# Kernel optimization log

Hardware: AMD Instinct MI355X
Metric: run time of the kernel (lower is better)

The kernel has to match this reference:

```python
import jax, jax.numpy as jnp
import numpy as np

GROUPS = 32
EPS = 1e-5


def _group_norm(x, w, b):
    B, C, H, W = x.shape
    xr = x.reshape(B, GROUPS, C // GROUPS, H, W)
    mean = xr.mean(axis=(2, 3, 4), keepdims=True)
    var = xr.var(axis=(2, 3, 4), keepdims=True)
    xn = ((xr - mean) * jax.lax.rsqrt(var + EPS)).reshape(B, C, H, W)
    return xn * w[None, :, None, None] + b[None, :, None, None]


def _conv1x1(w, b, x):
    # 1x1 conv == per-pixel channel matmul
    return jnp.einsum('oc,bchw->bohw', w, x) + b[None, :, None, None]


def setup_inputs() -> dict:
    key = jax.random.key(0)
    ks = jax.random.split(key, 6)
    C = 512
    s = 1.0 / np.sqrt(C)  # kaiming-uniform-ish scale for 1x1 convs
    return {
        'x': jax.random.normal(ks[0], (4, C, 64, 64), jnp.float32),
        'gn_w': jnp.ones((C,), jnp.float32),
        'gn_b': jnp.zeros((C,), jnp.float32),
        'qw': jax.random.normal(ks[1], (C, C), jnp.float32) * s,
        'qb': jnp.zeros((C,), jnp.float32),
        'kw': jax.random.normal(ks[2], (C, C), jnp.float32) * s,
        'kb': jnp.zeros((C,), jnp.float32),
        'vw': jax.random.normal(ks[3], (C, C), jnp.float32) * s,
        'vb': jnp.zeros((C,), jnp.float32),
        'pw': jax.random.normal(ks[4], (C, C), jnp.float32) * s,
        'pb': jnp.zeros((C,), jnp.float32),
    }


def reference(x, gn_w, gn_b, qw, qb, kw, kb, vw, vb, pw, pb):
    B, C, H, W = x.shape
    h_ = _group_norm(x, gn_w, gn_b)
    q = _conv1x1(qw, qb, h_).reshape(B, C, H * W)
    k = _conv1x1(kw, kb, h_).reshape(B, C, H * W)
    v = _conv1x1(vw, vb, h_).reshape(B, C, H * W)
    # scores [B, HW(query), HW(key)]
    scores = jnp.einsum('bcq,bck->bqk', q, k) * (C ** -0.5)
    attn = jax.nn.softmax(scores, axis=-1)
    out = jnp.einsum('bqk,bdk->bdq', attn, v).reshape(B, C, H, W)
    return x + _conv1x1(pw, pb, out)
```

## Files before the change

kernel.cpp:

```cpp
#include <hip/hip_runtime.h>

#define DEV __device__ __forceinline__

typedef __attribute__((ext_vector_type(8))) short short8;
typedef __attribute__((ext_vector_type(4))) float floatx4;
typedef __attribute__((ext_vector_type(4))) int i32x4;
typedef __attribute__((ext_vector_type(2))) long longx2;

DEV unsigned short f2bs(float x) {
    unsigned u = __float_as_uint(x);
    unsigned r = (u + 0x7fffu + ((u >> 16) & 1u)) >> 16;
    return (unsigned short)r;
}

DEV unsigned char f2fp8(float x) {
#if __has_builtin(__builtin_amdgcn_cvt_pk_fp8_f32)
    int pk = __builtin_amdgcn_cvt_pk_fp8_f32(x, 0.f, 0, false);
    return (unsigned char)(pk & 0xff);
#else
    unsigned u = __float_as_uint(x);
    unsigned s = (u >> 24) & 0x80;
    unsigned a = u & 0x7fffffff;
    unsigned um = a + 0x7ffffu + ((a >> 20) & 1u);
    unsigned r = (a >= 0x3c800000u) ? ((um >> 20) - 0x3C0u) : 0u;
    return (unsigned char)(r | s);
#endif
}

DEV unsigned pack_fp8x4(float v0, float v1, float v2, float v3) {
#if __has_builtin(__builtin_amdgcn_cvt_pk_fp8_f32)
    unsigned pk = (unsigned)__builtin_amdgcn_cvt_pk_fp8_f32(v0, v1, 0, false);
    pk = (unsigned)__builtin_amdgcn_cvt_pk_fp8_f32(v2, v3, (int)pk, true);
    return pk;
#else
    return (unsigned)f2fp8(v0) | ((unsigned)f2fp8(v1) << 8) |
           ((unsigned)f2fp8(v2) << 16) | ((unsigned)f2fp8(v3) << 24);
#endif
}

DEV unsigned pack_i8x4(float v0, float v1, float v2, float v3) {
    unsigned b0 = (unsigned)((int)rintf(v0)) & 255u;
    unsigned b1 = (unsigned)((int)rintf(v1)) & 255u;
    unsigned b2 = (unsigned)((int)rintf(v2)) & 255u;
    unsigned b3 = (unsigned)((int)rintf(v3)) & 255u;
    return b0 | (b1 << 8) | (b2 << 16) | (b3 << 24);
}

__global__ void pre_kernel(const float* __restrict__ x,
                           const float* __restrict__ qw, const float* __restrict__ kw,
                           const float* __restrict__ vw, const float* __restrict__ pw,
                           const float* __restrict__ qb, const float* __restrict__ kb,
                           unsigned short* __restrict__ wqkb, unsigned short* __restrict__ wvb,
                           unsigned short* __restrict__ wpb,
                           float* __restrict__ biasqk, float* __restrict__ rowsum,
                           float* __restrict__ stats) {
    int b = blockIdx.x, tid = threadIdx.x;
    if (b < 768) {
        const float* src = (b < 256) ? qw : (b < 512) ? kw : vw;
        unsigned short* dst = (b < 256) ? wqkb : (b < 512) ? (wqkb + 262144) : wvb;
        int off = (b & 255) * 256 + tid;
        float4 v = ((const float4*)src)[off];
        ushort4 o;
        o.x = f2bs(v.x); o.y = f2bs(v.y); o.z = f2bs(v.z); o.w = f2bs(v.w);
        ((ushort4*)dst)[off] = o;
    } else if (b < 1024) {
        int off = (b - 768) * 256 + tid;
        int row = off >> 7, c4 = (off & 127) * 4;
        float4 v = ((const float4*)pw)[off];
        float vv[4] = {v.x, v.y, v.z, v.w};
#pragma unroll
        for (int e = 0; e < 4; ++e) {
            int c = c4 + e;
            int j = (c >> 4) & 3, lc = c & 15;
            int cp = (c & ~63) | (lc * 4 + j);
            wpb[row * 512 + cp] = f2bs(vv[e]);
        }
    } else if (b == 1024) {
        biasqk[tid]       = qb[tid];
        biasqk[256 + tid] = qb[256 + tid];
        biasqk[512 + tid] = kb[tid];
        biasqk[768 + tid] = kb[256 + tid];
        float4 z = {0.f, 0.f, 0.f, 0.f};
#pragma unroll
        for (int k = 0; k < 16; ++k) ((float4*)rowsum)[k * 256 + tid] = z;
    } else {
        int bg = b - 1025;
        const float4* p = (const float4*)(x + (size_t)bg * 65536);
        float s = 0.f, ss = 0.f;
        for (int i = tid; i < 16384; i += 256) {
            float4 v = p[i];
            s += v.x + v.y + v.z + v.w;
            ss += v.x * v.x + v.y * v.y + v.z * v.z + v.w * v.w;
        }
        for (int off = 32; off; off >>= 1) { s += __shfl_down(s, off); ss += __shfl_down(ss, off); }
        __shared__ float rs[4], rss[4];
        int wave = tid >> 6, lane = tid & 63;
        if (lane == 0) { rs[wave] = s; rss[wave] = ss; }
        __syncthreads();
        if (tid == 0) {
            float S = rs[0] + rs[1] + rs[2] + rs[3];
            float SS = rss[0] + rss[1] + rss[2] + rss[3];
            float mean = S * (1.f / 65536.f);
            float var = SS * (1.f / 65536.f) - mean * mean;
            stats[bg * 2] = mean;
            stats[bg * 2 + 1] = rsqrtf(var + 1e-5f);
        }
    }
}

__global__ void gn_apply_kernel(const float* __restrict__ x, const float* __restrict__ stats,
                                const float* __restrict__ gw, const float* __restrict__ gb,
                                unsigned short* __restrict__ ht) {
    __shared__ __align__(16) unsigned short t[64][72];
    int b = blockIdx.z, c0 = blockIdx.y * 64, p0 = blockIdx.x * 64;
    int tid = threadIdx.x;
    const float* xb = x + ((size_t)b * 512 + c0) * 4096 + p0;
#pragma unroll
    for (int pass = 0; pass < 4; ++pass) {
        int cl = pass * 16 + (tid >> 4);
        int pq = (tid & 15) * 4;
        float4 v = *(const float4*)(xb + (size_t)cl * 4096 + pq);
        int c = c0 + cl, g = c >> 4;
        float mean = stats[(b * 32 + g) * 2], rstd = stats[(b * 32 + g) * 2 + 1];
        float sw = gw[c] * rstd;
        float sb = gb[c] - mean * sw;
        t[pq + 0][cl] = f2bs(v.x * sw + sb);
        t[pq + 1][cl] = f2bs(v.y * sw + sb);
        t[pq + 2][cl] = f2bs(v.z * sw + sb);
        t[pq + 3][cl] = f2bs(v.w * sw + sb);
    }
    __syncthreads();
    unsigned short* hb = ht + ((size_t)b * 4096 + p0) * 512 + c0;
#pragma unroll
    for (int pass = 0; pass < 2; ++pass) {
        int pl = pass * 32 + (tid >> 3);
        int c8 = (tid & 7) * 8;
        *(uint4*)(hb + (size_t)pl * 512 + c8) = *(const uint4*)&t[pl][c8];
    }
}

__global__ void gemm_qkv(const unsigned short* __restrict__ h_t, long long sP,
                         const unsigned short* __restrict__ wqkb,
                         const unsigned short* __restrict__ wvb,
                         char* __restrict__ q_i8, char* __restrict__ k_i8,
                         char* __restrict__ v_f8,
                         const float* __restrict__ biasqk, const float* __restrict__ vb,
                         float qs) {
    __shared__ __align__(16) unsigned short lA[128 * 64];
    __shared__ __align__(16) unsigned short lB[128 * 64];
    const int tid = threadIdx.x;
    const int wave = tid >> 6, lane = tid & 63;
    const int flat = blockIdx.x;
    const bool isqk = flat < 1024;
    int m0, n0, bz;
    const unsigned short *Ab, *Bb;
    if (isqk) {
        m0 = ((flat >> 3) & 31) * 128;
        n0 = (flat & 7) * 128;
        bz = flat >> 8;
        Ab = h_t + (size_t)bz * sP;
        Bb = wqkb;
    } else {
        const int g = flat - 1024;
        m0 = ((g >> 5) & 3) * 128;
        n0 = (g & 31) * 128;
        bz = g >> 7;
        Ab = wvb;
        Bb = h_t + (size_t)bz * sP;
    }

    floatx4 acc[4][4];
#pragma unroll
    for (int i = 0; i < 4; i++)
#pragma unroll
        for (int j = 0; j < 4; j++) acc[i][j] = (floatx4){0.f, 0.f, 0.f, 0.f};

    const int wm = (wave >> 1) * 64, wn = (wave & 1) * 64;
    const int quad = lane >> 4;
    const int lc = lane & 15;
    const int lc7 = lc & 7;

    for (int kt = 0; kt < 8; ++kt) {
        const int kbase = kt * 64;
#pragma unroll
        for (int c = 0; c < 4; ++c) {
            int d = c * 256 + tid;
            int r = d >> 3;
            int kc = (d & 7) ^ (r & 7);
            const unsigned short* ga = Ab + (size_t)(m0 + r) * 512 + kbase + kc * 8;
            const unsigned short* gb = Bb + (size_t)(n0 + r) * 512 + kbase + kc * 8;
            __builtin_amdgcn_global_load_lds(
                (const __attribute__((address_space(1))) void*)ga,
                (__attribute__((address_space(3))) void*)&lA[(size_t)(c * 256 + wave * 64) * 8], 16, 0, 0);
            __builtin_amdgcn_global_load_lds(
                (const __attribute__((address_space(1))) void*)gb,
                (__attribute__((address_space(3))) void*)&lB[(size_t)(c * 256 + wave * 64) * 8], 16, 0, 0);
        }
        __syncthreads();
#pragma unroll
        for (int kk = 0; kk < 2; ++kk) {
            const int swz = ((kk * 4 + quad) ^ lc7) * 8;
            short8 af[4], bf[4];
#pragma unroll
            for (int i = 0; i < 4; i++)
                af[i] = *(const short8*)&lA[(size_t)(wm + i * 16 + lc) * 64 + swz];
#pragma unroll
            for (int j = 0; j < 4; j++)
                bf[j] = *(const short8*)&lB[(size_t)(wn + j * 16 + lc) * 64 + swz];
#pragma unroll
            for (int i = 0; i < 4; i++)
#pragma unroll
                for (int j = 0; j < 4; j++)
                    acc[i][j] = __builtin_amdgcn_mfma_f32_16x16x32_bf16(af[i], bf[j], acc[i][j], 0, 0, 0);
        }
        __syncthreads();
    }

    const int rowb = quad * 4;
    if (isqk) {
#pragma unroll
        for (int i = 0; i < 4; i++) {
#pragma unroll
            for (int r = 0; r < 4; r++) {
                const int m = m0 + wm + i * 16 + rowb + r;
                float q[4];
#pragma unroll
                for (int j = 0; j < 4; j++) {
                    const int n = n0 + wn + j * 16 + lc;
                    q[j] = fminf(fmaxf((acc[i][j][r] + biasqk[n]) * qs, -127.f), 127.f);
                }
                const int col64 = n0 + wn;
                char* outp = (col64 < 512) ? q_i8 : k_i8;
                size_t idx = (size_t)bz * sP + (size_t)m * 512 +
                             (col64 - ((col64 < 512) ? 0 : 512)) + lc * 4;
                *(unsigned*)(outp + idx) = pack_i8x4(q[0], q[1], q[2], q[3]);
            }
        }
    } else {
#pragma unroll
        for (int i = 0; i < 4; i++) {
#pragma unroll
            for (int r = 0; r < 4; r++) {
                const int m = m0 + wm + i * 16 + rowb + r;
                const float bm = vb[m];
                float q[4];
#pragma unroll
                for (int j = 0; j < 4; j++)
                    q[j] = fminf(fmaxf(acc[i][j][r] + bm, -448.f), 448.f);
                size_t idx = (size_t)bz * sP + (size_t)m * 4096 + n0 + wn + lc * 4;
                *(unsigned*)(v_f8 + idx) = pack_fp8x4(q[0], q[1], q[2], q[3]);
            }
        }
    }
}

__global__ void gemm_proj(const unsigned short* __restrict__ A,
                          const unsigned short* __restrict__ B, long long sBb,
                          float* __restrict__ Cv, long long sCb,
                          const float* __restrict__ bias,
                          const float* __restrict__ resid, long long sRb,
                          int M, int N, int K) {
    __shared__ __align__(16) unsigned short lA[128 * 64];
    __shared__ __align__(16) unsigned short lB[128 * 64];
    const int tid = threadIdx.x;
    const int wave = tid >> 6, lane = tid & 63;
    const int m0 = blockIdx.y * 128, n0 = blockIdx.x * 128, bz = blockIdx.z;
    const unsigned short* Ab = A;
    const unsigned short* Bb = B + (size_t)bz * sBb;

    floatx4 acc[4][4];
#pragma unroll
    for (int i = 0; i < 4; i++)
#pragma unroll
        for (int j = 0; j < 4; j++) acc[i][j] = (floatx4){0.f, 0.f, 0.f, 0.f};

    const int wm = (wave >> 1) * 64, wn = (wave & 1) * 64;
    const int quad = lane >> 4;
    const int lc = lane & 15;
    const int lc7 = lc & 7;

    const int nk = K >> 6;
    for (int kt = 0; kt < nk; ++kt) {
        const int kbase = kt * 64;
#pragma unroll
        for (int c = 0; c < 4; ++c) {
            int d = c * 256 + tid;
            int r = d >> 3;
            int kc = (d & 7) ^ (r & 7);
            const unsigned short* ga = Ab + (size_t)(m0 + r) * K + kbase + kc * 8;
            const unsigned short* gb = Bb + (size_t)(n0 + r) * K + kbase + kc * 8;
            __builtin_amdgcn_global_load_lds(
                (const __attribute__((address_space(1))) void*)ga,
                (__attribute__((address_space(3))) void*)&lA[(size_t)(c * 256 + wave * 64) * 8], 16, 0, 0);
            __builtin_amdgcn_global_load_lds(
                (const __attribute__((address_space(1))) void*)gb,
                (__attribute__((address_space(3))) void*)&lB[(size_t)(c * 256 + wave * 64) * 8], 16, 0, 0);
        }
        __syncthreads();
#pragma unroll
        for (int kk = 0; kk < 2; ++kk) {
            const int swz = ((kk * 4 + quad) ^ lc7) * 8;
            short8 af[4], bf[4];
#pragma unroll
            for (int i = 0; i < 4; i++)
                af[i] = *(const short8*)&lA[(size_t)(wm + i * 16 + lc) * 64 + swz];
#pragma unroll
            for (int j = 0; j < 4; j++)
                bf[j] = *(const short8*)&lB[(size_t)(wn + j * 16 + lc) * 64 + swz];
#pragma unroll
            for (int i = 0; i < 4; i++)
#pragma unroll
                for (int j = 0; j < 4; j++)
                    acc[i][j] = __builtin_amdgcn_mfma_f32_16x16x32_bf16(af[i], bf[j], acc[i][j], 0, 0, 0);
        }
        __syncthreads();
    }

    const int rowb = quad * 4;
#pragma unroll
    for (int i = 0; i < 4; i++) {
#pragma unroll
        for (int r = 0; r < 4; r++) {
            const int m = m0 + wm + i * 16 + rowb + r;
            const float bm = bias[m];
#pragma unroll
            for (int j = 0; j < 4; j++) {
                const int n = n0 + wn + j * 16 + lc;
                size_t idx = (size_t)bz * sCb + (size_t)m * N + n;
                Cv[idx] = acc[i][j][r] + bm + resid[(size_t)bz * sRb + (size_t)m * N + n];
            }
        }
    }
}

__global__ void gemm_i8_exp(const char* __restrict__ A, long long sAb,
                            const char* __restrict__ B, long long sBb,
                            char* __restrict__ Cv, long long sCb,
                            float* __restrict__ rowsum,
                            int M, int N, int K, float scale2) {
    __shared__ __align__(16) char lA[128 * 128];
    __shared__ __align__(16) char lB[128 * 128];
    const int tid = threadIdx.x;
    const int wave = tid >> 6, lane = tid & 63;
    const int m0 = blockIdx.y * 128, n0 = blockIdx.x * 128, bz = blockIdx.z;
    const char* Ab = A + (size_t)bz * sAb;
    const char* Bb = B + (size_t)bz * sBb;

    i32x4 acc[4][4];
#pragma unroll
    for (int i = 0; i < 4; i++)
#pragma unroll
        for (int j = 0; j < 4; j++) acc[i][j] = (i32x4){0, 0, 0, 0};

    const int wm = (wave >> 1) * 64, wn = (wave & 1) * 64;
    const int quad = lane >> 4;
    const int lc = lane & 15;
    const int lc7 = lc & 7;

    const int nk = K >> 7;
    for (int kt = 0; kt < nk; ++kt) {
        const int kbase = kt * 128;
#pragma unroll
        for (int c = 0; c < 4; ++c) {
            int d = c * 256 + tid;
            int r = d >> 3;
            int kc = (d & 7) ^ (r & 7);
            const char* ga = Ab + (size_t)(m0 + r) * K + kbase + kc * 16;
            const char* gb = Bb + (size_t)(n0 + r) * K + kbase + kc * 16;
            __builtin_amdgcn_global_load_lds(
                (const __attribute__((address_space(1))) void*)ga,
                (__attribute__((address_space(3))) void*)&lA[(size_t)(c * 256 + wave * 64) * 16], 16, 0, 0);
            __builtin_amdgcn_global_load_lds(
                (const __attribute__((address_space(1))) void*)gb,
                (__attribute__((address_space(3))) void*)&lB[(size_t)(c * 256 + wave * 64) * 16], 16, 0, 0);
        }
        __syncthreads();
#pragma unroll
        for (int kk = 0; kk < 2; ++kk) {
            const int swz = ((kk * 4 + quad) ^ lc7) * 16;
            i32x4 af[4], bf[4];
#pragma unroll
            for (int i = 0; i < 4; i++)
                af[i] = *(const i32x4*)&lA[(size_t)(wm + i * 16 + lc) * 128 + swz];
#pragma unroll
            for (int j = 0; j < 4; j++)
                bf[j] = *(const i32x4*)&lB[(size_t)(wn + j * 16 + lc) * 128 + swz];
#pragma unroll
            for (int i = 0; i < 4; i++)
#pragma unroll
                for (int j = 0; j < 4; j++)
                    acc[i][j] = __builtin_amdgcn_mfma_i32_16x16x64_i8(af[i], bf[j], acc[i][j], 0, 0, 0);
        }
        __syncthreads();
    }

    const int rowb = quad * 4;
#pragma unroll
    for (int i = 0; i < 4; i++) {
#pragma unroll
        for (int r = 0; r < 4; r++) {
            const int m = m0 + wm + i * 16 + rowb + r;
            float e[4];
            float rsacc = 0.f;
#pragma unroll
            for (int j = 0; j < 4; j++) {
                e[j] = fminf(exp2f(fmaf((float)acc[i][j][r], scale2, -2.0f)), 448.f);
                rsacc += e[j];
            }
            size_t oidx = (size_t)bz * sCb + (size_t)m * N + n0 + wn + lc * 4;
            *(unsigned*)(Cv + oidx) = pack_fp8x4(e[0], e[1], e[2], e[3]);
            rsacc += __shfl_xor(rsacc, 1);
            rsacc += __shfl_xor(rsacc, 2);
            rsacc += __shfl_xor(rsacc, 4);
            rsacc += __shfl_xor(rsacc, 8);
            if (lc == 0) atomicAdd(&rowsum[(size_t)bz * M + m], rsacc);
        }
    }
}

__global__ void gemm_fp8_o(const char* __restrict__ A, long long sAb,
                           const char* __restrict__ B, long long sBb,
                           unsigned short* __restrict__ Cv, long long sCb,
                           const float* __restrict__ rowsum,
                           int M, int N, int K) {
    __shared__ __align__(16) char lA[128 * 128];
    __shared__ __align__(16) char lB[128 * 128];
    const int tid = threadIdx.x;
    const int wave = tid >> 6, lane = tid & 63;
    int flat = blockIdx.x;
    int xcd = flat & 7, idx = flat >> 3;
    int nt = idx & 3, si = idx >> 2;
    int stripe = xcd * 16 + si;
    const int m0 = (stripe & 31) * 128;
    const int n0 = nt * 128;
    const int bz = stripe >> 5;
    const char* Ab = A + (size_t)bz * sAb;
    const char* Bb = B + (size_t)bz * sBb;

    floatx4 acc[4][4];
#pragma unroll
    for (int i = 0; i < 4; i++)
#pragma unroll
        for (int j = 0; j < 4; j++) acc[i][j] = (floatx4){0.f, 0.f, 0.f, 0.f};

    const int wm = (wave >> 1) * 64, wn = (wave & 1) * 64;
    const int quad = lane >> 4;
    const int lc = lane & 15;
    const int lc7 = lc & 7;
    const int half = quad & 1;

    const int nk = K >> 7;
    for (int kt = 0; kt < nk; ++kt) {
        const int kbase = kt * 128;
#pragma unroll
        for (int c = 0; c < 4; ++c) {
            int d = c * 256 + tid;
            int r = d >> 3;
            int kc = (d & 7) ^ (r & 7);
            const char* ga = Ab + (size_t)(m0 + r) * K + kbase + kc * 16;
            const char* gb = Bb + (size_t)(n0 + r) * K + kbase + kc * 16;
            __builtin_amdgcn_global_load_lds(
                (const __attribute__((address_space(1))) void*)ga,
                (__attribute__((address_space(3))) void*)&lA[(size_t)(c * 256 + wave * 64) * 16], 16, 0, 0);
            __builtin_amdgcn_global_load_lds(
                (const __attribute__((address_space(1))) void*)gb,
                (__attribute__((address_space(3))) void*)&lB[(size_t)(c * 256 + wave * 64) * 16], 16, 0, 0);
        }
        __syncthreads();
#pragma unroll
        for (int t = 0; t < 4; ++t) {
            const int swz = ((2 * t + (quad >> 1)) ^ lc7) * 16;
            long a8[4], b8[4];
#pragma unroll
            for (int i = 0; i < 4; i++) {
                longx2 v = *(const longx2*)&lA[(size_t)(wm + i * 16 + lc) * 128 + swz];
                a8[i] = v[half];
            }
#pragma unroll
            for (int j = 0; j < 4; j++) {
                longx2 v = *(const longx2*)&lB[(size_t)(wn + j * 16 + lc) * 128 + swz];
                b8[j] = v[half];
            }
#pragma unroll
            for (int i = 0; i < 4; i++)
#pragma unroll
                for (int j = 0; j < 4; j++)
                    acc[i][j] = __builtin_amdgcn_mfma_f32_16x16x32_fp8_fp8(a8[i], b8[j], acc[i][j], 0, 0, 0);
        }
        __syncthreads();
    }

    const int rowb = quad * 4;
#pragma unroll
    for (int i = 0; i < 4; i++) {
#pragma unroll
        for (int r = 0; r < 4; r++) {
            const int m = m0 + wm + i * 16 + rowb + r;
            const float pscale = 1.f / rowsum[(size_t)bz * M + m];
            unsigned short h[4];
#pragma unroll
            for (int j = 0; j < 4; j++) h[j] = f2bs(acc[i][j][r] * pscale);
            uint2 u;
            u.x = (unsigned)h[0] | ((unsigned)h[1] << 16);
            u.y = (unsigned)h[2] | ((unsigned)h[3] << 16);
            *(uint2*)&Cv[(size_t)bz * sCb + (size_t)m * N + n0 + wn + lc * 4] = u;
        }
    }
}

extern "C" void kernel_launch(void* const* d_in, const int* in_sizes, int n_in,
                              void* d_out, int out_size, void* d_ws, size_t ws_size,
                              hipStream_t stream) {
    (void)in_sizes; (void)n_in; (void)out_size; (void)ws_size;
    const float* x   = (const float*)d_in[0];
    const float* gnw = (const float*)d_in[1];
    const float* gnb = (const float*)d_in[2];
    const float* qw  = (const float*)d_in[3];
    const float* qb  = (const float*)d_in[4];
    const float* kw  = (const float*)d_in[5];
    const float* kb  = (const float*)d_in[6];
    const float* vw  = (const float*)d_in[7];
    const float* vb  = (const float*)d_in[8];
    const float* pw  = (const float*)d_in[9];
    const float* pb  = (const float*)d_in[10];
    float* out = (float*)d_out;

    char* ws = (char*)d_ws;
    unsigned short* h_t = (unsigned short*)(ws);
    unsigned short* o_t = h_t;
    char* q_i8 = (char*)(ws + (16ull << 20));
    char* k_i8 = (char*)(ws + (32ull << 20));
    char* v_f8 = (char*)(ws + (48ull << 20));
    unsigned short* wqkb = (unsigned short*)(ws + (64ull << 20));
    unsigned short* wvb = (unsigned short*)(ws + (65ull << 20));
    unsigned short* wpb = wvb + 262144;
    float* stats  = (float*)(ws + (66ull << 20));
    float* rowsum = (float*)(ws + (66ull << 20) + 65536);
    float* biasqk = (float*)(ws + (66ull << 20) + 131072);
    char* p_f8 = (char*)(ws + (67ull << 20));

    const long long sP  = 2097152;
    const long long sS  = 16777216;
    const float QS = 16.f;
    const float SC = 0.044194173824159216f / (QS * QS);
    const float LOG2E = 1.4426950408889634f;

    pre_kernel<<<1153, 256, 0, stream>>>(x, qw, kw, vw, pw, qb, kb, wqkb, wvb, wpb,
                                         biasqk, rowsum, stats);
    gn_apply_kernel<<<dim3(64, 8, 4), 256, 0, stream>>>(x, stats, gnw, gnb, h_t);
    gemm_qkv<<<1536, 256, 0, stream>>>(h_t, sP, wqkb, wvb, q_i8, k_i8, v_f8, biasqk, vb, QS);
    gemm_i8_exp<<<dim3(32, 32, 4), 256, 0, stream>>>(q_i8, sP, k_i8, sP, p_f8, sS, rowsum,
                                                     4096, 4096, 512, SC * LOG2E);
    gemm_fp8_o<<<dim3(512, 1, 1), 256, 0, stream>>>(p_f8, sS, v_f8, sP, o_t, sP, rowsum,
                                                    4096, 512, 4096);
    gemm_proj<<<dim3(32, 4, 4), 256, 0, stream>>>(wpb, o_t, sP, out, sP, pb, x, sP,
                                                  512, 4096, 512);
}
```

Measured before the change: 312.3 us.

## Enlarge QK^T int8 GEMM tile to 256x256 with double-buffered LDS staging

The score GEMM with fused exp moves from 128x128 tiles on 256 threads to 256x256 tiles on 512 threads, with each wave computing a 128x64 sub-tile. Global-to-LDS loads are double-buffered so the next K slice is fetched while the current one feeds the MFMAs, and s_setprio raises wave priority around the MFMA block. This targets operand reuse and hides load latency, at the cost of 128KB of LDS and more accumulator registers per thread, which cuts occupancy and leaves only 1024 blocks.

```diff
diff --git a/kernel.cpp b/kernel.cpp
--- a/kernel.cpp
+++ b/kernel.cpp
@@ -333,79 +333,89 @@
     }
 }
 
-__global__ void gemm_i8_exp(const char* __restrict__ A, long long sAb,
+__global__ __launch_bounds__(512) void gemm_i8_exp(const char* __restrict__ A, long long sAb,
                             const char* __restrict__ B, long long sBb,
                             char* __restrict__ Cv, long long sCb,
                             float* __restrict__ rowsum,
                             int M, int N, int K, float scale2) {
-    __shared__ __align__(16) char lA[128 * 128];
-    __shared__ __align__(16) char lB[128 * 128];
+    __shared__ __align__(16) char lA[2][256 * 128];
+    __shared__ __align__(16) char lB[2][256 * 128];
     const int tid = threadIdx.x;
     const int wave = tid >> 6, lane = tid & 63;
-    const int m0 = blockIdx.y * 128, n0 = blockIdx.x * 128, bz = blockIdx.z;
+    const int m0 = blockIdx.y * 256, n0 = blockIdx.x * 256, bz = blockIdx.z;
     const char* Ab = A + (size_t)bz * sAb;
     const char* Bb = B + (size_t)bz * sBb;
 
-    i32x4 acc[4][4];
-#pragma unroll
-    for (int i = 0; i < 4; i++)
+    i32x4 acc[8][4];
+#pragma unroll
+    for (int i = 0; i < 8; i++)
 #pragma unroll
         for (int j = 0; j < 4; j++) acc[i][j] = (i32x4){0, 0, 0, 0};
 
-    const int wm = (wave >> 1) * 64, wn = (wave & 1) * 64;
+    const int wm = (wave >> 2) * 128, wn = (wave & 3) * 64;
     const int quad = lane >> 4;
     const int lc = lane & 15;
     const int lc7 = lc & 7;
 
+    auto stage = [&](char* dA, char* dB, int kbase) {
+#pragma unroll
+        for (int c = 0; c < 4; ++c) {
+            int d = c * 512 + tid;
+            int r = d >> 3;
+            int s = ((d & 7) ^ (r & 7)) * 16;
+            const char* ga = Ab + (size_t)(m0 + r) * K + kbase + s;
+            const char* gb = Bb + (size_t)(n0 + r) * K + kbase + s;
+            __builtin_amdgcn_global_load_lds(
+                (const __attribute__((address_space(1))) void*)ga,
+                (__attribute__((address_space(3))) void*)(dA + (size_t)(c * 512 + wave * 64) * 16), 16, 0, 0);
+            __builtin_amdgcn_global_load_lds(
+                (const __attribute__((address_space(1))) void*)gb,
+                (__attribute__((address_space(3))) void*)(dB + (size_t)(c * 512 + wave * 64) * 16), 16, 0, 0);
+        }
+    };
+
     const int nk = K >> 7;
+    stage(lA[0], lB[0], 0);
+    __syncthreads();
+    int buf = 0;
     for (int kt = 0; kt < nk; ++kt) {
-        const int kbase = kt * 128;
-#pragma unroll
-        for (int c = 0; c < 4; ++c) {
-            int d = c * 256 + tid;
-            int r = d >> 3;
-            int kc = (d & 7) ^ (r & 7);
-            const char* ga = Ab + (size_t)(m0 + r) * K + kbase + kc * 16;
-            const char* gb = Bb + (size_t)(n0 + r) * K + kbase + kc * 16;
-            __builtin_amdgcn_global_load_lds(
-                (const __attribute__((address_space(1))) void*)ga,
-                (__attribute__((address_space(3))) void*)&lA[(size_t)(c * 256 + wave * 64) * 16], 16, 0, 0);
-            __builtin_amdgcn_global_load_lds(
-                (const __attribute__((address_space(1))) void*)gb,
-                (__attribute__((address_space(3))) void*)&lB[(size_t)(c * 256 + wave * 64) * 16], 16, 0, 0);
-        }
-        __syncthreads();
+        if (kt + 1 < nk) stage(lA[buf ^ 1], lB[buf ^ 1], (kt + 1) << 7);
+        const char* pa = lA[buf];
+        const char* pb = lB[buf];
 #pragma unroll
         for (int kk = 0; kk < 2; ++kk) {
-            const int swz = ((kk * 4 + quad) ^ lc7) * 16;
-            i32x4 af[4], bf[4];
-#pragma unroll
-            for (int i = 0; i < 4; i++)
-                af[i] = *(const i32x4*)&lA[(size_t)(wm + i * 16 + lc) * 128 + swz];
-#pragma unroll
-            for (int j = 0; j < 4; j++)
-                bf[j] = *(const i32x4*)&lB[(size_t)(wn + j * 16 + lc) * 128 + swz];
-#pragma unroll
-            for (int i = 0; i < 4; i++)
-#pragma unroll
-                for (int j = 0; j < 4; j++)
-                    acc[i][j] = __builtin_amdgcn_mfma_i32_16x16x64_i8(af[i], bf[j], acc[i][j], 0, 0, 0);
-        }
-        __syncthreads();
+            i32x4 bf[4];
+#pragma unroll
+            for (int fj = 0; fj < 4; ++fj)
+                bf[fj] = *(const i32x4*)&pb[(size_t)(wn + fj * 16 + lc) * 128 +
+                                            (((kk * 4 + quad) ^ lc7) << 4)];
+            __builtin_amdgcn_s_setprio(1);
+#pragma unroll
+            for (int fi = 0; fi < 8; ++fi) {
+                i32x4 a = *(const i32x4*)&pa[(size_t)(wm + fi * 16 + lc) * 128 +
+                                             (((kk * 4 + quad) ^ lc7) << 4)];
+#pragma unroll
+                for (int fj = 0; fj < 4; ++fj)
+                    acc[fi][fj] = __builtin_amdgcn_mfma_i32_16x16x64_i8(a, bf[fj], acc[fi][fj], 0, 0, 0);
+            }
+            __builtin_amdgcn_s_setprio(0);
+        }
+        __syncthreads();
+        buf ^= 1;
     }
 
     const int rowb = quad * 4;
 #pragma unroll
-    for (int i = 0; i < 4; i++) {
-#pragma unroll
-        for (int r = 0; r < 4; r++) {
-            const int m = m0 + wm + i * 16 + rowb + r;
+    for (int fi = 0; fi < 8; ++fi) {
+#pragma unroll
+        for (int r = 0; r < 4; ++r) {
+            const int m = m0 + wm + fi * 16 + rowb + r;
             float e[4];
             float rsacc = 0.f;
 #pragma unroll
-            for (int j = 0; j < 4; j++) {
-                e[j] = fminf(exp2f(fmaf((float)acc[i][j][r], scale2, -2.0f)), 448.f);
-                rsacc += e[j];
+            for (int fj = 0; fj < 4; ++fj) {
+                e[fj] = fminf(exp2f(fmaf((float)acc[fi][fj][r], scale2, -2.0f)), 448.f);
+                rsacc += e[fj];
             }
             size_t oidx = (size_t)bz * sCb + (size_t)m * N + n0 + wn + lc * 4;
             *(unsigned*)(Cv + oidx) = pack_fp8x4(e[0], e[1], e[2], e[3]);
@@ -549,7 +559,7 @@
                                          biasqk, rowsum, stats);
     gn_apply_kernel<<<dim3(64, 8, 4), 256, 0, stream>>>(x, stats, gnw, gnb, h_t);
     gemm_qkv<<<1536, 256, 0, stream>>>(h_t, sP, wqkb, wvb, q_i8, k_i8, v_f8, biasqk, vb, QS);
-    gemm_i8_exp<<<dim3(32, 32, 4), 256, 0, stream>>>(q_i8, sP, k_i8, sP, p_f8, sS, rowsum,
+    gemm_i8_exp<<<dim3(16, 16, 4), 512, 0, stream>>>(q_i8, sP, k_i8, sP, p_f8, sS, rowsum,
                                                      4096, 4096, 512, SC * LOG2E);
     gemm_fp8_o<<<dim3(512, 1, 1), 256, 0, stream>>>(p_f8, sS, v_f8, sP, o_t, sP, rowsum,
                                                     4096, 512, 4096);
```

After: 318.6 us. About the same (+2.0%).

## Fuse QK^T, exp and PV into a flash-style split-KV attention kernel

Applied to the files above, without the earlier changes.

Replaces the separate int8 score GEMM (which wrote a full 4096x4096 fp8 probability matrix per batch) and the fp8 PV GEMM with a single fused kernel. That kernel keeps Q resident in LDS, streams K and V tiles, computes exp scores into LDS and accumulates the output directly. The KV range is split in two and each half writes its unnormalized output and row sums. The projection GEMM then reduces over the concatenated halves (K=1024) and applies the 1/rowsum normalisation, removing the large P round trip to global memory and the rowsum atomics. The fused kernel has only 256 blocks of 512 threads and little pipelining between K/V loads and MFMA, so occupancy and latency hiding are risks.

```diff
diff --git a/kernel.cpp b/kernel.cpp
--- a/kernel.cpp
+++ b/kernel.cpp
@@ -46,13 +46,20 @@
     return b0 | (b1 << 8) | (b2 << 16) | (b3 << 24);
 }
 
+DEV void syncfull() {
+    asm volatile("s_waitcnt vmcnt(0) lgkmcnt(0)" ::: "memory");
+    __builtin_amdgcn_sched_barrier(0);
+    __builtin_amdgcn_s_barrier();
+    __builtin_amdgcn_sched_barrier(0);
+}
+
 __global__ void pre_kernel(const float* __restrict__ x,
                            const float* __restrict__ qw, const float* __restrict__ kw,
                            const float* __restrict__ vw, const float* __restrict__ pw,
                            const float* __restrict__ qb, const float* __restrict__ kb,
                            unsigned short* __restrict__ wqkb, unsigned short* __restrict__ wvb,
                            unsigned short* __restrict__ wpb,
-                           float* __restrict__ biasqk, float* __restrict__ rowsum,
+                           float* __restrict__ biasqk,
                            float* __restrict__ stats) {
     int b = blockIdx.x, tid = threadIdx.x;
     if (b < 768) {
@@ -80,9 +87,6 @@
         biasqk[256 + tid] = qb[256 + tid];
         biasqk[512 + tid] = kb[tid];
         biasqk[768 + tid] = kb[256 + tid];
-        float4 z = {0.f, 0.f, 0.f, 0.f};
-#pragma unroll
-        for (int k = 0; k < 16; ++k) ((float4*)rowsum)[k * 256 + tid] = z;
     } else {
         int bg = b - 1025;
         const float4* p = (const float4*)(x + (size_t)bg * 65536);
@@ -254,11 +258,172 @@
     }
 }
 
+__global__ __launch_bounds__(512, 2) void attn_fused(
+    const char* __restrict__ Qg, const char* __restrict__ Kg,
+    const char* __restrict__ Vg,
+    unsigned short* __restrict__ Ou, long long sOb,
+    float* __restrict__ rsum, float scale2) {
+    __shared__ __align__(16) char Ql[128 * 512];
+    __shared__ __align__(16) char Kl[64 * 512];
+    __shared__ __align__(16) char Vl[512 * 64];
+    __shared__ __align__(16) char Pl[128 * 64];
+    const int tid = threadIdx.x;
+    const int wave = tid >> 6, lane = tid & 63;
+    const int quad = lane >> 4, lc = lane & 15;
+    const int id = blockIdx.x;
+    const int xcd = id & 7, qi = id >> 3;
+    const int bz = xcd >> 1, split = xcd & 1;
+    const int q0 = qi * 128;
+    const int kvbase = split * 2048;
+    const int NIT = 32;
+
+    const char* Qb = Qg + ((size_t)bz * 4096 + q0) * 512;
+    const char* Kb = Kg + ((size_t)bz * 4096 + kvbase) * 512;
+    const char* Vb = Vg + (size_t)bz * 2097152 + kvbase;
+
+    const int wq = wave * 16;
+    const int mO = (wave >> 2) * 64, nO = (wave & 3) * 128;
+
+    auto stageQ = [&]() {
+#pragma unroll
+        for (int c = 0; c < 8; ++c) {
+            int f = c * 512 + tid;
+            int r = f >> 5, g = f & 31;
+            int gs = (g & 24) | ((g & 7) ^ (r & 7));
+            __builtin_amdgcn_global_load_lds(
+                (const __attribute__((address_space(1))) void*)(Qb + (size_t)r * 512 + gs * 16),
+                (__attribute__((address_space(3))) void*)(Ql + (size_t)f * 16), 16, 0, 0);
+        }
+    };
+    auto stageK = [&](int t) {
+#pragma unroll
+        for (int c = 0; c < 4; ++c) {
+            int f = c * 512 + tid;
+            int r = f >> 5, g = f & 31;
+            int gs = (g & 24) | ((g & 7) ^ (r & 7));
+            __builtin_amdgcn_global_load_lds(
+                (const __attribute__((address_space(1))) void*)(Kb + (size_t)(t * 64 + r) * 512 + gs * 16),
+                (__attribute__((address_space(3))) void*)(Kl + (size_t)f * 16), 16, 0, 0);
+        }
+    };
+    auto stageV = [&](int t) {
+#pragma unroll
+        for (int c = 0; c < 4; ++c) {
+            int f = c * 512 + tid;
+            int r = f >> 2, g = f & 3;
+            int gs = g ^ (r & 3);
+            __builtin_amdgcn_global_load_lds(
+                (const __attribute__((address_space(1))) void*)(Vb + (size_t)r * 4096 + t * 64 + gs * 16),
+                (__attribute__((address_space(3))) void*)(Vl + (size_t)f * 16), 16, 0, 0);
+        }
+    };
+
+    floatx4 acco[4][8];
+#pragma unroll
+    for (int i = 0; i < 4; ++i)
+#pragma unroll
+        for (int j = 0; j < 8; ++j) acco[i][j] = (floatx4){0.f, 0.f, 0.f, 0.f};
+    float rs = 0.f;
+
+    stageQ();
+    stageK(0);
+    stageV(0);
+    syncfull();
+
+    const int q = wq + lc;
+    const int q7 = q & 7;
+
+    for (int t = 0; t < NIT; ++t) {
+        if (t > 0) stageV(t);
+        i32x4 accs[4];
+#pragma unroll
+        for (int ki = 0; ki < 4; ++ki) accs[ki] = (i32x4){0, 0, 0, 0};
+#pragma unroll
+        for (int ks = 0; ks < 8; ++ks) {
+            const int g = ks * 4 + quad;
+            i32x4 bfrag = *(const i32x4*)&Ql[(size_t)q * 512 +
+                                             (((g & 24) | ((g & 7) ^ q7)) << 4)];
+#pragma unroll
+            for (int ki = 0; ki < 4; ++ki) {
+                const int ar = ki * 16 + lc;
+                i32x4 afrag = *(const i32x4*)&Kl[(size_t)ar * 512 +
+                                                 (((g & 24) | ((g & 7) ^ (ar & 7))) << 4)];
+                accs[ki] = __builtin_amdgcn_mfma_i32_16x16x64_i8(afrag, bfrag, accs[ki], 0, 0, 0);
+            }
+        }
+        float e[4][4];
+#pragma unroll
+        for (int ki = 0; ki < 4; ++ki)
+#pragma unroll
+            for (int r = 0; r < 4; ++r) {
+                e[ki][r] = fminf(exp2f(fmaf((float)accs[ki][r], scale2, -2.0f)), 448.f);
+                rs += e[ki][r];
+            }
+#pragma unroll
+        for (int r = 0; r < 4; ++r) {
+            unsigned w = pack_fp8x4(e[0][r], e[1][r], e[2][r], e[3][r]);
+            const int s4 = quad * 4 + r;
+            const int byte = q * 64 + (((s4 >> 1) ^ q7) << 3) + ((s4 & 1) << 2);
+            *(unsigned*)&Pl[byte] = w;
+        }
+        syncfull();
+
+        if (t + 1 < NIT) stageK(t + 1);
+#pragma unroll
+        for (int ks2 = 0; ks2 < 2; ++ks2) {
+            long pa[4], vf[8];
+#pragma unroll
+            for (int i = 0; i < 4; ++i) {
+                const int row = mO + i * 16 + lc;
+                pa[i] = *(const long*)&Pl[(size_t)row * 64 +
+                                          (((ks2 * 4 + quad) ^ (row & 7)) << 3)];
+            }
+#pragma unroll
+            for (int j = 0; j < 8; ++j) {
+                const int row = nO + j * 16 + lc;
+                const int g16 = ks2 * 2 + (quad >> 1);
+                vf[j] = *(const long*)&Vl[(size_t)row * 64 +
+                                          ((g16 ^ (row & 3)) << 4) + ((quad & 1) << 3)];
+            }
+#pragma unroll
+            for (int i = 0; i < 4; ++i)
+#pragma unroll
+                for (int j = 0; j < 8; ++j)
+                    acco[i][j] = __builtin_amdgcn_mfma_f32_16x16x32_fp8_fp8(pa[i], vf[j], acco[i][j], 0, 0, 0);
+        }
+        syncfull();
+    }
+
+    rs += __shfl_xor(rs, 16);
+    rs += __shfl_xor(rs, 32);
+    if (quad == 0) rsum[((size_t)(split * 4 + bz)) * 4096 + q0 + q] = rs;
+
+#pragma unroll
+    for (int i = 0; i < 4; ++i) {
+#pragma unroll
+        for (int r = 0; r < 4; ++r) {
+            const int m = q0 + mO + i * 16 + quad * 4 + r;
+            unsigned short h[8];
+#pragma unroll
+            for (int j = 0; j < 8; ++j) h[j] = f2bs(acco[i][j][r]);
+            unsigned short* base = Ou + (size_t)bz * sOb + (size_t)m * 1024 + split * 512 + nO;
+            uint2 u0, u1;
+            u0.x = (unsigned)h[0] | ((unsigned)h[1] << 16);
+            u0.y = (unsigned)h[2] | ((unsigned)h[3] << 16);
+            u1.x = (unsigned)h[4] | ((unsigned)h[5] << 16);
+            u1.y = (unsigned)h[6] | ((unsigned)h[7] << 16);
+            *(uint2*)(base + lc * 4) = u0;
+            *(uint2*)(base + 64 + lc * 4) = u1;
+        }
+    }
+}
+
 __global__ void gemm_proj(const unsigned short* __restrict__ A,
                           const unsigned short* __restrict__ B, long long sBb,
                           float* __restrict__ Cv, long long sCb,
                           const float* __restrict__ bias,
                           const float* __restrict__ resid, long long sRb,
+                          const float* __restrict__ rsum,
                           int M, int N, int K) {
     __shared__ __align__(16) unsigned short lA[128 * 64];
     __shared__ __align__(16) unsigned short lB[128 * 64];
@@ -287,8 +452,8 @@
             int d = c * 256 + tid;
             int r = d >> 3;
             int kc = (d & 7) ^ (r & 7);
-            const unsigned short* ga = Ab + (size_t)(m0 + r) * K + kbase + kc * 8;
-            const unsigned short* gb = Bb + (size_t)(n0 + r) * K + kbase + kc * 8;
+            const unsigned short* ga = Ab + (size_t)(m0 + r) * 512 + ((kbase & 511) + kc * 8);
+            const unsigned short* gb = Bb + (size_t)(n0 + r) * 1024 + kbase + kc * 8;
             __builtin_amdgcn_global_load_lds(
                 (const __attribute__((address_space(1))) void*)ga,
                 (__attribute__((address_space(3))) void*)&lA[(size_t)(c * 256 + wave * 64) * 8], 16, 0, 0);
@@ -316,6 +481,13 @@
         __syncthreads();
     }
 
+    float rsinv[4];
+#pragma unroll
+    for (int j = 0; j < 4; j++) {
+        const int n = n0 + wn + j * 16 + lc;
+        rsinv[j] = 1.f / (rsum[(size_t)bz * 4096 + n] + rsum[(size_t)(4 + bz) * 4096 + n]);
+    }
+
     const int rowb = quad * 4;
 #pragma unroll
     for (int i = 0; i < 4; i++) {
@@ -327,183 +499,8 @@
             for (int j = 0; j < 4; j++) {
                 const int n = n0 + wn + j * 16 + lc;
                 size_t idx = (size_t)bz * sCb + (size_t)m * N + n;
-                Cv[idx] = acc[i][j][r] + bm + resid[(size_t)bz * sRb + (size_t)m * N + n];
-            }
-        }
-    }
-}
-
-__global__ void gemm_i8_exp(const char* __restrict__ A, long long sAb,
-                            const char* __restrict__ B, long long sBb,
-                            char* __restrict__ Cv, long long sCb,
-                            float* __restrict__ rowsum,
-                            int M, int N, int K, float scale2) {
-    __shared__ __align__(16) char lA[128 * 128];
-    __shared__ __align__(16) char lB[128 * 128];
-    const int tid = threadIdx.x;
-    const int wave = tid >> 6, lane = tid & 63;
-    const int m0 = blockIdx.y * 128, n0 = blockIdx.x * 128, bz = blockIdx.z;
-    const char* Ab = A + (size_t)bz * sAb;
-    const char* Bb = B + (size_t)bz * sBb;
-
-    i32x4 acc[4][4];
-#pragma unroll
-    for (int i = 0; i < 4; i++)
-#pragma unroll
-        for (int j = 0; j < 4; j++) acc[i][j] = (i32x4){0, 0, 0, 0};
-
-    const int wm = (wave >> 1) * 64, wn = (wave & 1) * 64;
-    const int quad = lane >> 4;
-    const int lc = lane & 15;
-    const int lc7 = lc & 7;
-
-    const int nk = K >> 7;
-    for (int kt = 0; kt < nk; ++kt) {
-        const int kbase = kt * 128;
-#pragma unroll
-        for (int c = 0; c < 4; ++c) {
-            int d = c * 256 + tid;
-            int r = d >> 3;
-            int kc = (d & 7) ^ (r & 7);
-            const char* ga = Ab + (size_t)(m0 + r) * K + kbase + kc * 16;
-            const char* gb = Bb + (size_t)(n0 + r) * K + kbase + kc * 16;
-            __builtin_amdgcn_global_load_lds(
-                (const __attribute__((address_space(1))) void*)ga,
-                (__attribute__((address_space(3))) void*)&lA[(size_t)(c * 256 + wave * 64) * 16], 16, 0, 0);
-            __builtin_amdgcn_global_load_lds(
-                (const __attribute__((address_space(1))) void*)gb,
-                (__attribute__((address_space(3))) void*)&lB[(size_t)(c * 256 + wave * 64) * 16], 16, 0, 0);
-        }
-        __syncthreads();
-#pragma unroll
-        for (int kk = 0; kk < 2; ++kk) {
-            const int swz = ((kk * 4 + quad) ^ lc7) * 16;
-            i32x4 af[4], bf[4];
-#pragma unroll
-            for (int i = 0; i < 4; i++)
-                af[i] = *(const i32x4*)&lA[(size_t)(wm + i * 16 + lc) * 128 + swz];
-#pragma unroll
-            for (int j = 0; j < 4; j++)
-                bf[j] = *(const i32x4*)&lB[(size_t)(wn + j * 16 + lc) * 128 + swz];
-#pragma unroll
-            for (int i = 0; i < 4; i++)
-#pragma unroll
-                for (int j = 0; j < 4; j++)
-                    acc[i][j] = __builtin_amdgcn_mfma_i32_16x16x64_i8(af[i], bf[j], acc[i][j], 0, 0, 0);
-        }
-        __syncthreads();
-    }
-
-    const int rowb = quad * 4;
-#pragma unroll
-    for (int i = 0; i < 4; i++) {
-#pragma unroll
-        for (int r = 0; r < 4; r++) {
-            const int m = m0 + wm + i * 16 + rowb + r;
-            float e[4];
-            float rsacc = 0.f;
-#pragma unroll
-            for (int j = 0; j < 4; j++) {
-                e[j] = fminf(exp2f(fmaf((float)acc[i][j][r], scale2, -2.0f)), 448.f);
-                rsacc += e[j];
-            }
-            size_t oidx = (size_t)bz * sCb + (size_t)m * N + n0 + wn + lc * 4;
-            *(unsigned*)(Cv + oidx) = pack_fp8x4(e[0], e[1], e[2], e[3]);
-            rsacc += __shfl_xor(rsacc, 1);
-            rsacc += __shfl_xor(rsacc, 2);
-            rsacc += __shfl_xor(rsacc, 4);
-            rsacc += __shfl_xor(rsacc, 8);
-            if (lc == 0) atomicAdd(&rowsum[(size_t)bz * M + m], rsacc);
-        }
-    }
-}
-
-__global__ void gemm_fp8_o(const char* __restrict__ A, long long sAb,
-                           const char* __restrict__ B, long long sBb,
-                           unsigned short* __restrict__ Cv, long long sCb,
-                           const float* __restrict__ rowsum,
-                           int M, int N, int K) {
-    __shared__ __align__(16) char lA[128 * 128];
-    __shared__ __align__(16) char lB[128 * 128];
-    const int tid = threadIdx.x;
-    const int wave = tid >> 6, lane = tid & 63;
-    int flat = blockIdx.x;
-    int xcd = flat & 7, idx = flat >> 3;
-    int nt = idx & 3, si = idx >> 2;
-    int stripe = xcd * 16 + si;
-    const int m0 = (stripe & 31) * 128;
-    const int n0 = nt * 128;
-    const int bz = stripe >> 5;
-    const char* Ab = A + (size_t)bz * sAb;
-    const char* Bb = B + (size_t)bz * sBb;
-
-    floatx4 acc[4][4];
-#pragma unroll
-    for (int i = 0; i < 4; i++)
-#pragma unroll
-        for (int j = 0; j < 4; j++) acc[i][j] = (floatx4){0.f, 0.f, 0.f, 0.f};
-
-    const int wm = (wave >> 1) * 64, wn = (wave & 1) * 64;
-    const int quad = lane >> 4;
-    const int lc = lane & 15;
-    const int lc7 = lc & 7;
-    const int half = quad & 1;
-
-    const int nk = K >> 7;
-    for (int kt = 0; kt < nk; ++kt) {
-        const int kbase = kt * 128;
-#pragma unroll
-        for (int c = 0; c < 4; ++c) {
-            int d = c * 256 + tid;
-            int r = d >> 3;
-            int kc = (d & 7) ^ (r & 7);
-            const char* ga = Ab + (size_t)(m0 + r) * K + kbase + kc * 16;
-            const char* gb = Bb + (size_t)(n0 + r) * K + kbase + kc * 16;
-            __builtin_amdgcn_global_load_lds(
-                (const __attribute__((address_space(1))) void*)ga,
-                (__attribute__((address_space(3))) void*)&lA[(size_t)(c * 256 + wave * 64) * 16], 16, 0, 0);
-            __builtin_amdgcn_global_load_lds(
-                (const __attribute__((address_space(1))) void*)gb,
-                (__attribute__((address_space(3))) void*)&lB[(size_t)(c * 256 + wave * 64) * 16], 16, 0, 0);
-        }
-        __syncthreads();
-#pragma unroll
-        for (int t = 0; t < 4; ++t) {
-            const int swz = ((2 * t + (quad >> 1)) ^ lc7) * 16;
-            long a8[4], b8[4];
-#pragma unroll
-            for (int i = 0; i < 4; i++) {
-                longx2 v = *(const longx2*)&lA[(size_t)(wm + i * 16 + lc) * 128 + swz];
-                a8[i] = v[half];
-            }
-#pragma unroll
-            for (int j = 0; j < 4; j++) {
-                longx2 v = *(const longx2*)&lB[(size_t)(wn + j * 16 + lc) * 128 + swz];
-                b8[j] = v[half];
-            }
-#pragma unroll
-            for (int i = 0; i < 4; i++)
-#pragma unroll
-                for (int j = 0; j < 4; j++)
-                    acc[i][j] = __builtin_amdgcn_mfma_f32_16x16x32_fp8_fp8(a8[i], b8[j], acc[i][j], 0, 0, 0);
-        }
-        __syncthreads();
-    }
-
-    const int rowb = quad * 4;
-#pragma unroll
-    for (int i = 0; i < 4; i++) {
-#pragma unroll
-        for (int r = 0; r < 4; r++) {
-            const int m = m0 + wm + i * 16 + rowb + r;
-            const float pscale = 1.f / rowsum[(size_t)bz * M + m];
-            unsigned short h[4];
-#pragma unroll
-            for (int j = 0; j < 4; j++) h[j] = f2bs(acc[i][j][r] * pscale);
-            uint2 u;
-            u.x = (unsigned)h[0] | ((unsigned)h[1] << 16);
-            u.y = (unsigned)h[2] | ((unsigned)h[3] << 16);
-            *(uint2*)&Cv[(size_t)bz * sCb + (size_t)m * N + n0 + wn + lc * 4] = u;
+                Cv[idx] = acc[i][j][r] * rsinv[j] + bm + resid[(size_t)bz * sRb + (size_t)m * N + n];
+            }
         }
     }
 }
@@ -527,7 +524,6 @@
 
     char* ws = (char*)d_ws;
     unsigned short* h_t = (unsigned short*)(ws);
-    unsigned short* o_t = h_t;
     char* q_i8 = (char*)(ws + (16ull << 20));
     char* k_i8 = (char*)(ws + (32ull << 20));
     char* v_f8 = (char*)(ws + (48ull << 20));
@@ -535,24 +531,22 @@
     unsigned short* wvb = (unsigned short*)(ws + (65ull << 20));
     unsigned short* wpb = wvb + 262144;
     float* stats  = (float*)(ws + (66ull << 20));
+    float* biasqk = (float*)(ws + (66ull << 20) + 8192);
     float* rowsum = (float*)(ws + (66ull << 20) + 65536);
-    float* biasqk = (float*)(ws + (66ull << 20) + 131072);
-    char* p_f8 = (char*)(ws + (67ull << 20));
+    unsigned short* o_un = (unsigned short*)(ws + (72ull << 20));
 
     const long long sP  = 2097152;
-    const long long sS  = 16777216;
+    const long long sOb = 4194304;
     const float QS = 16.f;
     const float SC = 0.044194173824159216f / (QS * QS);
     const float LOG2E = 1.4426950408889634f;
 
     pre_kernel<<<1153, 256, 0, stream>>>(x, qw, kw, vw, pw, qb, kb, wqkb, wvb, wpb,
-                                         biasqk, rowsum, stats);
+                                         biasqk, stats);
     gn_apply_kernel<<<dim3(64, 8, 4), 256, 0, stream>>>(x, stats, gnw, gnb, h_t);
     gemm_qkv<<<1536, 256, 0, stream>>>(h_t, sP, wqkb, wvb, q_i8, k_i8, v_f8, biasqk, vb, QS);
-    gemm_i8_exp<<<dim3(32, 32, 4), 256, 0, stream>>>(q_i8, sP, k_i8, sP, p_f8, sS, rowsum,
-                                                     4096, 4096, 512, SC * LOG2E);
-    gemm_fp8_o<<<dim3(512, 1, 1), 256, 0, stream>>>(p_f8, sS, v_f8, sP, o_t, sP, rowsum,
-                                                    4096, 512, 4096);
-    gemm_proj<<<dim3(32, 4, 4), 256, 0, stream>>>(wpb, o_t, sP, out, sP, pb, x, sP,
-                                                  512, 4096, 512);
-}
+    attn_fused<<<dim3(256), 512, 0, stream>>>(q_i8, k_i8, v_f8, o_un, sOb, rowsum,
+                                              SC * LOG2E);
+    gemm_proj<<<dim3(32, 4, 4), 256, 0, stream>>>(wpb, o_un, sOb, out, sP, pb, x, sP,
+                                                  rowsum, 512, 4096, 1024);
+}
```

After: 313.6 us. No clear change (+0.4%).
